# Optimization experiments

Hardware: AMD Instinct MI355X
Metric: run time of the kernel (lower is better)

## Reference

```python
import jax, jax.numpy as jnp
import numpy as np

SIGMA_DIS = 3.0
MAX_LABELS = 33  # label ids in [0, 32]; 0 = background, 1..32 = kernels


def setup_inputs() -> dict:
    key = jax.random.key(0)
    k1, k2 = jax.random.split(key)
    B, C, H, W = 8, 4, 896, 896
    pred = jax.random.normal(k1, (B, C, H, W), dtype=jnp.float32)
    kernels_mask = jnp.ones((B, H, W), dtype=jnp.float32)
    labels = jax.random.randint(k2, (B, H, W), 0, MAX_LABELS, dtype=jnp.int32)
    return {
        "pred_similarities": pred,
        "kernels_mask": kernels_mask,
        "kernel_mask_ndi_labels": labels,
    }


def _disc_loss(pred, labels, sigma):
    # pred: [B, C, H, W], labels: [B, H, W] int
    B, C = pred.shape[0], pred.shape[1]
    p = pred.reshape(B, C, -1)        # [B, C, N]
    lab = labels.reshape(B, -1)       # [B, N]

    # Masks for distinct labels are disjoint, so for a = pred*mask_i/|K_i|,
    # b = pred*mask_j/|K_j|:  ||a - b||_F^2 = s_i + s_j where
    # s_k = sum_{pixels in K_k} sum_c pred^2 / |K_k|^2.
    sq = jnp.sum(p * p, axis=1)       # [B, N]

    def seg(x, l):
        return jax.ops.segment_sum(x, l, num_segments=MAX_LABELS)

    card = jax.vmap(seg)(jnp.ones_like(sq), lab)   # [B, L] pixel counts
    ssq = jax.vmap(seg)(sq, lab)                   # [B, L] sum of squares
    safe_card = jnp.where(card > 0, card, 1.0)
    s = ssq / (safe_card * safe_card)              # [B, L]

    nk = jnp.max(lab, axis=1)                      # [B] num_kernels per image
    ks = jnp.arange(MAX_LABELS)
    valid = (ks[None, :] >= 1) & (ks[None, :] <= nk[:, None]) & (card > 0)  # [B, L]

    # all unordered pairs i < j of valid labels
    pair_mask = (
        valid[:, :, None] & valid[:, None, :] & (ks[:, None] < ks[None, :])[None]
    )  # [B, L, L]
    S = s[:, :, None] + s[:, None, :]
    S_safe = jnp.where(pair_mask, S, 1.0)          # keep sqrt grads finite
    # NOTE: original torch.max(norm, 0)[0] on a 0-d tensor is a dim-reduction
    # over a size-1 view and is an identity, NOT a clamp; replicated faithfully.
    d = sigma - jnp.sqrt(S_safe)
    term = jnp.log(d * d + 1.0)
    per_b = jnp.sum(jnp.where(pair_mask, term, 0.0), axis=(1, 2))  # [B]

    nk_f = nk.astype(per_b.dtype)
    denom = jnp.where(nk > 1, nk_f * (nk_f - 1.0), 1.0)
    loss_b = jnp.where(nk > 1, per_b / denom, 0.0)
    return jnp.sum(loss_b)


def reference(pred_similarities, kernels_mask, kernel_mask_ndi_labels):
    # kernels_mask is reshaped but never used by the original forward math.
    return _disc_loss(pred_similarities, kernel_mask_ndi_labels, SIGMA_DIS)
```

## Files before the change

kernel.cpp:

```cpp
#include <hip/hip_runtime.h>

#define MAXL 33
#define CSTR 36
#define PB 128
#define TPB 128
#define GSTR (PB * TPB)

__global__ __launch_bounds__(TPB, 2) void seg_hist_kernel(
    const float* __restrict__ pred, const int* __restrict__ labels,
    float* __restrict__ partial, int N) {
  const int b = blockIdx.y;
  const int ng = N >> 2;
  __shared__ float sumh[TPB * MAXL];
  __shared__ unsigned char cnth[TPB * CSTR];
  __shared__ float xred[2][2][MAXL];
  const int tid = threadIdx.x;

  float* sh = &sumh[tid * MAXL];
  unsigned char* ch = &cnth[tid * CSTR];
#pragma unroll
  for (int i = 0; i < MAXL; ++i) sh[i] = 0.f;
#pragma unroll
  for (int i = 0; i < CSTR / 4; ++i) reinterpret_cast<unsigned*>(ch)[i] = 0u;

  const float4* p = reinterpret_cast<const float4*>(pred) + (size_t)b * 4 * ng;
  const int4* lb = reinterpret_cast<const int4*>(labels) + (size_t)b * ng;
  const int start = blockIdx.x * TPB + tid;
  const bool has13 = (start + 12 * GSTR) < ng;

  auto ld = [&](int g, float4& c0, float4& c1, float4& c2, float4& c3,
                int4& l) {
    c0 = p[g];
    c1 = p[g + ng];
    c2 = p[g + 2 * ng];
    c3 = p[g + 3 * ng];
    l = lb[g];
  };
  auto proc = [&](const float4& c0, const float4& c1, const float4& c2,
                  const float4& c3, const int4& l) {
    float s0 = c0.x * c0.x + c1.x * c1.x + c2.x * c2.x + c3.x * c3.x;
    float s1 = c0.y * c0.y + c1.y * c1.y + c2.y * c2.y + c3.y * c3.y;
    float s2 = c0.z * c0.z + c1.z * c1.z + c2.z * c2.z + c3.z * c3.z;
    float s3 = c0.w * c0.w + c1.w * c1.w + c2.w * c2.w + c3.w * c3.w;
    const bool e01 = l.x == l.y, e02 = l.x == l.z, e03 = l.x == l.w;
    const bool e12 = l.y == l.z, e13 = l.y == l.w, e23 = l.z == l.w;
    const float w1 = s1 + (e01 ? s0 : 0.f);
    const float w2 = s2 + (e12 ? s1 : 0.f) + (e02 ? s0 : 0.f);
    const float w3 =
        s3 + (e23 ? s2 : 0.f) + (e13 ? s1 : 0.f) + (e03 ? s0 : 0.f);
    const unsigned m1 = 1u + (unsigned)e01;
    const unsigned m2 = 1u + (unsigned)e12 + (unsigned)e02;
    const unsigned m3 = 1u + (unsigned)e23 + (unsigned)e13 + (unsigned)e03;
    const float r0 = sh[l.x], r1 = sh[l.y], r2 = sh[l.z], r3 = sh[l.w];
    const unsigned q0 = ch[l.x], q1 = ch[l.y], q2 = ch[l.z], q3 = ch[l.w];
    sh[l.x] = r0 + s0;
    sh[l.y] = r1 + w1;
    sh[l.z] = r2 + w2;
    sh[l.w] = r3 + w3;
    ch[l.x] = (unsigned char)(q0 + 1u);
    ch[l.y] = (unsigned char)(q1 + m1);
    ch[l.z] = (unsigned char)(q2 + m2);
    ch[l.w] = (unsigned char)(q3 + m3);
  };

  float4 A0, A1, A2, A3, B0, B1, B2, B3, C0, C1, C2, C3;
  int4 Al, Bl, Cl;

  ld(start + 0 * GSTR, A0, A1, A2, A3, Al);
  ld(start + 1 * GSTR, B0, B1, B2, B3, Bl);
  ld(start + 2 * GSTR, C0, C1, C2, C3, Cl);

#pragma unroll
  for (int k = 0; k < 3; ++k) {
    proc(A0, A1, A2, A3, Al);
    ld(start + (3 * k + 3) * GSTR, A0, A1, A2, A3, Al);
    proc(B0, B1, B2, B3, Bl);
    ld(start + (3 * k + 4) * GSTR, B0, B1, B2, B3, Bl);
    proc(C0, C1, C2, C3, Cl);
    ld(start + (3 * k + 5) * GSTR, C0, C1, C2, C3, Cl);
  }
  proc(A0, A1, A2, A3, Al);
  if (has13) ld(start + 12 * GSTR, A0, A1, A2, A3, Al);
  proc(B0, B1, B2, B3, Bl);
  proc(C0, C1, C2, C3, Cl);
  if (has13) proc(A0, A1, A2, A3, Al);
  __syncthreads();

  const int wave = tid >> 6;
  const int lane = tid & 63;
  if (lane < MAXL) {
    float fs = 0.f;
    unsigned fc = 0u;
#pragma unroll 8
    for (int u = 0; u < 64; ++u) {
      fs += sumh[(wave * 64 + u) * MAXL + lane];
      fc += (unsigned)cnth[(wave * 64 + u) * CSTR + lane];
    }
    xred[wave][0][lane] = fs;
    xred[wave][1][lane] = (float)fc;
  }
  __syncthreads();
  if (tid < MAXL) {
    partial[(size_t)(b * 2 * MAXL + tid) * PB + blockIdx.x] =
        xred[0][0][tid] + xred[1][0][tid];
    partial[(size_t)(b * 2 * MAXL + MAXL + tid) * PB + blockIdx.x] =
        xred[0][1][tid] + xred[1][1][tid];
  }
}

__global__ __launch_bounds__(512) void reduce_finalize_kernel(
    const float* __restrict__ partial, float* __restrict__ out) {
  __shared__ float red[8 * 2 * MAXL];
  __shared__ float s_val[8 * MAXL];
  __shared__ float s_flag[8 * MAXL];
  __shared__ float s_invden[8];
  __shared__ float s_part[8];
  const int tid = threadIdx.x;
  const int wave = tid >> 6;
  const int lane = tid & 63;

  {
    int slot = tid;
    const float4* row =
        reinterpret_cast<const float4*>(partial) + (size_t)slot * (PB / 4);
    float a0 = 0.f, a1 = 0.f;
#pragma unroll 8
    for (int u = 0; u < PB / 4; u += 2) {
      float4 x = row[u], y = row[u + 1];
      a0 += x.x + x.y + x.z + x.w;
      a1 += y.x + y.y + y.z + y.w;
    }
    if (slot < 8 * 2 * MAXL) red[slot] = a0 + a1;
  }
  if (tid < 8 * 2 * MAXL - 512) {
    int slot = 512 + tid;
    const float4* row =
        reinterpret_cast<const float4*>(partial) + (size_t)slot * (PB / 4);
    float a0 = 0.f, a1 = 0.f;
#pragma unroll 8
    for (int u = 0; u < PB / 4; u += 2) {
      float4 x = row[u], y = row[u + 1];
      a0 += x.x + x.y + x.z + x.w;
      a1 += y.x + y.y + y.z + y.w;
    }
    red[slot] = a0 + a1;
  }
  __syncthreads();

  for (int i = tid; i < 8 * MAXL; i += 512) {
    int b = i / MAXL, l = i - b * MAXL;
    float cnt = red[b * 2 * MAXL + MAXL + l];
    float ssq = red[b * 2 * MAXL + l];
    float safe = cnt > 0.f ? cnt : 1.f;
    s_val[i] = ssq / (safe * safe);
    s_flag[i] = (l >= 1 && cnt > 0.f) ? 1.f : 0.f;
  }
  __syncthreads();
  if (tid < 8) {
    int nk = 0;
    for (int l = MAXL - 1; l >= 0; --l) {
      if (red[tid * 2 * MAXL + MAXL + l] > 0.f) {
        nk = l;
        break;
      }
    }
    s_invden[tid] = (nk > 1) ? 1.f / ((float)nk * ((float)nk - 1.f)) : 0.f;
  }
  __syncthreads();

  float local = 0.f;
  const int total = 8 * MAXL * MAXL;
  for (int idx = tid; idx < total; idx += 512) {
    int b = idx / (MAXL * MAXL);
    int r = idx - b * MAXL * MAXL;
    int i = r / MAXL;
    int j = r - i * MAXL;
    if (i < j && s_flag[b * MAXL + i] != 0.f && s_flag[b * MAXL + j] != 0.f) {
      float S = s_val[b * MAXL + i] + s_val[b * MAXL + j];
      float d = 3.0f - sqrtf(S);
      local += logf(d * d + 1.f) * s_invden[b];
    }
  }
  for (int off = 32; off; off >>= 1) local += __shfl_down(local, off, 64);
  if (lane == 0) s_part[wave] = local;
  __syncthreads();
  if (tid == 0) {
    float tot = 0.f;
    for (int w = 0; w < 8; ++w) tot += s_part[w];
    out[0] = tot;
  }
}

extern "C" void kernel_launch(void* const* d_in, const int* in_sizes, int n_in,
                              void* d_out, int out_size, void* d_ws,
                              size_t ws_size, hipStream_t stream) {
  const float* pred = (const float*)d_in[0];
  const int* labels = (const int*)d_in[2];
  float* out = (float*)d_out;

  const int B = 8;
  const int N = in_sizes[2] / B;

  float* partial = (float*)d_ws;

  dim3 grid(PB, B);
  seg_hist_kernel<<<grid, dim3(TPB), 0, stream>>>(pred, labels, partial, N);
  reduce_finalize_kernel<<<dim3(1), dim3(512), 0, stream>>>(partial, out);
}
```

Measured before the change: 39.58 us.

## Transpose per-thread shared histograms to bin-major layout and reshape partials

Per-thread histograms move from a thread-major layout (stride 33 floats plus byte counters) to a bin-major [bin][thread] layout with 32-bit counters. Each thread's accesses then land in its own bank column, which avoids bank conflicts and byte read-modify-write. The cross-thread reduction now uses wave shuffles per bin, and the partials are stored in block-major order. The finalize kernel is rewritten to 576 threads, reads the partials with a strided pattern and computes s inline, dropping one barrier. The trade-offs are doubled shared memory for the counters and uncoalesced strided reads in the finalize kernel.

```diff
diff --git a/kernel.cpp b/kernel.cpp
--- a/kernel.cpp
+++ b/kernel.cpp
@@ -1,7 +1,7 @@
 #include <hip/hip_runtime.h>
 
 #define MAXL 33
-#define CSTR 36
+#define NSLOT 66
 #define PB 128
 #define TPB 128
 #define GSTR (PB * TPB)
@@ -11,17 +11,19 @@
     float* __restrict__ partial, int N) {
   const int b = blockIdx.y;
   const int ng = N >> 2;
-  __shared__ float sumh[TPB * MAXL];
-  __shared__ unsigned char cnth[TPB * CSTR];
-  __shared__ float xred[2][2][MAXL];
+  __shared__ float sumh[MAXL][TPB];
+  __shared__ unsigned cnth[MAXL][TPB];
+  __shared__ float xr[NSLOT];
   const int tid = threadIdx.x;
 
-  float* sh = &sumh[tid * MAXL];
-  unsigned char* ch = &cnth[tid * CSTR];
-#pragma unroll
-  for (int i = 0; i < MAXL; ++i) sh[i] = 0.f;
-#pragma unroll
-  for (int i = 0; i < CSTR / 4; ++i) reinterpret_cast<unsigned*>(ch)[i] = 0u;
+  {
+    float* sf = &sumh[0][0];
+    unsigned* cf = &cnth[0][0];
+    for (int i = tid; i < MAXL * TPB; i += TPB) {
+      sf[i] = 0.f;
+      cf[i] = 0u;
+    }
+  }
 
   const float4* p = reinterpret_cast<const float4*>(pred) + (size_t)b * 4 * ng;
   const int4* lb = reinterpret_cast<const int4*>(labels) + (size_t)b * ng;
@@ -51,16 +53,18 @@
     const unsigned m1 = 1u + (unsigned)e01;
     const unsigned m2 = 1u + (unsigned)e12 + (unsigned)e02;
     const unsigned m3 = 1u + (unsigned)e23 + (unsigned)e13 + (unsigned)e03;
-    const float r0 = sh[l.x], r1 = sh[l.y], r2 = sh[l.z], r3 = sh[l.w];
-    const unsigned q0 = ch[l.x], q1 = ch[l.y], q2 = ch[l.z], q3 = ch[l.w];
-    sh[l.x] = r0 + s0;
-    sh[l.y] = r1 + w1;
-    sh[l.z] = r2 + w2;
-    sh[l.w] = r3 + w3;
-    ch[l.x] = (unsigned char)(q0 + 1u);
-    ch[l.y] = (unsigned char)(q1 + m1);
-    ch[l.z] = (unsigned char)(q2 + m2);
-    ch[l.w] = (unsigned char)(q3 + m3);
+    const float r0 = sumh[l.x][tid], r1 = sumh[l.y][tid];
+    const float r2 = sumh[l.z][tid], r3 = sumh[l.w][tid];
+    const unsigned q0 = cnth[l.x][tid], q1 = cnth[l.y][tid];
+    const unsigned q2 = cnth[l.z][tid], q3 = cnth[l.w][tid];
+    sumh[l.x][tid] = r0 + s0;
+    sumh[l.y][tid] = r1 + w1;
+    sumh[l.z][tid] = r2 + w2;
+    sumh[l.w][tid] = r3 + w3;
+    cnth[l.x][tid] = q0 + 1u;
+    cnth[l.y][tid] = q1 + m1;
+    cnth[l.z][tid] = q2 + m2;
+    cnth[l.w][tid] = q3 + m3;
   };
 
   float4 A0, A1, A2, A3, B0, B1, B2, B3, C0, C1, C2, C3;
@@ -88,78 +92,51 @@
 
   const int wave = tid >> 6;
   const int lane = tid & 63;
-  if (lane < MAXL) {
-    float fs = 0.f;
-    unsigned fc = 0u;
-#pragma unroll 8
-    for (int u = 0; u < 64; ++u) {
-      fs += sumh[(wave * 64 + u) * MAXL + lane];
-      fc += (unsigned)cnth[(wave * 64 + u) * CSTR + lane];
+  for (int bin = wave; bin < MAXL; bin += 2) {
+    float fs = sumh[bin][lane] + sumh[bin][64 + lane];
+    unsigned fc = cnth[bin][lane] + cnth[bin][64 + lane];
+    for (int off = 32; off; off >>= 1) {
+      fs += __shfl_down(fs, off, 64);
+      fc += __shfl_down(fc, off, 64);
     }
-    xred[wave][0][lane] = fs;
-    xred[wave][1][lane] = (float)fc;
+    if (lane == 0) {
+      xr[bin] = fs;
+      xr[MAXL + bin] = (float)fc;
+    }
   }
   __syncthreads();
-  if (tid < MAXL) {
-    partial[(size_t)(b * 2 * MAXL + tid) * PB + blockIdx.x] =
-        xred[0][0][tid] + xred[1][0][tid];
-    partial[(size_t)(b * 2 * MAXL + MAXL + tid) * PB + blockIdx.x] =
-        xred[0][1][tid] + xred[1][1][tid];
-  }
+  if (tid < NSLOT)
+    partial[(size_t)(b * PB + blockIdx.x) * NSLOT + tid] = xr[tid];
 }
 
-__global__ __launch_bounds__(512) void reduce_finalize_kernel(
+__global__ __launch_bounds__(576) void reduce_finalize_kernel(
     const float* __restrict__ partial, float* __restrict__ out) {
-  __shared__ float red[8 * 2 * MAXL];
-  __shared__ float s_val[8 * MAXL];
-  __shared__ float s_flag[8 * MAXL];
+  __shared__ float red[8 * NSLOT];
   __shared__ float s_invden[8];
-  __shared__ float s_part[8];
+  __shared__ float s_part[9];
   const int tid = threadIdx.x;
   const int wave = tid >> 6;
   const int lane = tid & 63;
 
-  {
-    int slot = tid;
-    const float4* row =
-        reinterpret_cast<const float4*>(partial) + (size_t)slot * (PB / 4);
-    float a0 = 0.f, a1 = 0.f;
+  if (tid < 8 * NSLOT) {
+    const int bb = tid / NSLOT, s = tid - bb * NSLOT;
+    const float* base = partial + (size_t)bb * PB * NSLOT + s;
+    float a0 = 0.f, a1 = 0.f, a2 = 0.f, a3 = 0.f;
 #pragma unroll 8
-    for (int u = 0; u < PB / 4; u += 2) {
-      float4 x = row[u], y = row[u + 1];
-      a0 += x.x + x.y + x.z + x.w;
-      a1 += y.x + y.y + y.z + y.w;
+    for (int blk = 0; blk < PB; blk += 4) {
+      a0 += base[(size_t)(blk + 0) * NSLOT];
+      a1 += base[(size_t)(blk + 1) * NSLOT];
+      a2 += base[(size_t)(blk + 2) * NSLOT];
+      a3 += base[(size_t)(blk + 3) * NSLOT];
     }
-    if (slot < 8 * 2 * MAXL) red[slot] = a0 + a1;
-  }
-  if (tid < 8 * 2 * MAXL - 512) {
-    int slot = 512 + tid;
-    const float4* row =
-        reinterpret_cast<const float4*>(partial) + (size_t)slot * (PB / 4);
-    float a0 = 0.f, a1 = 0.f;
-#pragma unroll 8
-    for (int u = 0; u < PB / 4; u += 2) {
-      float4 x = row[u], y = row[u + 1];
-      a0 += x.x + x.y + x.z + x.w;
-      a1 += y.x + y.y + y.z + y.w;
-    }
-    red[slot] = a0 + a1;
+    red[tid] = (a0 + a1) + (a2 + a3);
   }
   __syncthreads();
 
-  for (int i = tid; i < 8 * MAXL; i += 512) {
-    int b = i / MAXL, l = i - b * MAXL;
-    float cnt = red[b * 2 * MAXL + MAXL + l];
-    float ssq = red[b * 2 * MAXL + l];
-    float safe = cnt > 0.f ? cnt : 1.f;
-    s_val[i] = ssq / (safe * safe);
-    s_flag[i] = (l >= 1 && cnt > 0.f) ? 1.f : 0.f;
-  }
-  __syncthreads();
   if (tid < 8) {
     int nk = 0;
-    for (int l = MAXL - 1; l >= 0; --l) {
-      if (red[tid * 2 * MAXL + MAXL + l] > 0.f) {
+    for (int l = MAXL - 1; l >= 1; --l) {
+      if (red[tid * NSLOT + MAXL + l] > 0.f) {
         nk = l;
         break;
       }
@@ -170,15 +147,20 @@
 
   float local = 0.f;
   const int total = 8 * MAXL * MAXL;
-  for (int idx = tid; idx < total; idx += 512) {
-    int b = idx / (MAXL * MAXL);
-    int r = idx - b * MAXL * MAXL;
+  for (int idx = tid; idx < total; idx += 576) {
+    int bb = idx / (MAXL * MAXL);
+    int r = idx - bb * (MAXL * MAXL);
     int i = r / MAXL;
     int j = r - i * MAXL;
-    if (i < j && s_flag[b * MAXL + i] != 0.f && s_flag[b * MAXL + j] != 0.f) {
-      float S = s_val[b * MAXL + i] + s_val[b * MAXL + j];
-      float d = 3.0f - sqrtf(S);
-      local += logf(d * d + 1.f) * s_invden[b];
+    if (i >= 1 && i < j) {
+      float ci = red[bb * NSLOT + MAXL + i];
+      float cj = red[bb * NSLOT + MAXL + j];
+      if (ci > 0.f && cj > 0.f) {
+        float si = red[bb * NSLOT + i] / (ci * ci);
+        float sj = red[bb * NSLOT + j] / (cj * cj);
+        float d = 3.0f - sqrtf(si + sj);
+        local += logf(d * d + 1.f) * s_invden[bb];
+      }
     }
   }
   for (int off = 32; off; off >>= 1) local += __shfl_down(local, off, 64);
@@ -186,7 +168,7 @@
   __syncthreads();
   if (tid == 0) {
     float tot = 0.f;
-    for (int w = 0; w < 8; ++w) tot += s_part[w];
+    for (int w = 0; w < 9; ++w) tot += s_part[w];
     out[0] = tot;
   }
 }
@@ -205,5 +187,5 @@
 
   dim3 grid(PB, B);
   seg_hist_kernel<<<grid, dim3(TPB), 0, stream>>>(pred, labels, partial, N);
-  reduce_finalize_kernel<<<dim3(1), dim3(512), 0, stream>>>(partial, out);
+  reduce_finalize_kernel<<<dim3(1), dim3(576), 0, stream>>>(partial, out);
 }
```

Result: slower. 41.52 us (+4.9%).
